# Kernel optimization log

Hardware: AMD Instinct MI355X
Metric: run time of the kernel (lower is better)

## Reference

```python
import jax, jax.numpy as jnp
import numpy as np

EMBED_DIM = 1024
NUM_HEADS = 16
D_K = EMBED_DIM // NUM_HEADS
GAMMA = 1.0


def setup_inputs() -> dict:
    key = jax.random.key(0)
    ks = jax.random.split(key, 5)
    B, N, E = 2, 2048, EMBED_DIM
    scale = 1.0 / np.sqrt(E)
    x = jax.random.normal(ks[0], (B, N, E), dtype=jnp.float32)
    Wq = jax.random.normal(ks[1], (E, E), dtype=jnp.float32) * scale
    Wk = jax.random.normal(ks[2], (E, E), dtype=jnp.float32) * scale
    Wv = jax.random.normal(ks[3], (E, E), dtype=jnp.float32) * scale
    Wo = jax.random.normal(ks[4], (E, E), dtype=jnp.float32) * scale
    mask = jnp.ones((B, N), dtype=jnp.int32)
    return {"x": x, "Wq": Wq, "Wk": Wk, "Wv": Wv, "Wo": Wo, "mask": mask}


def _split_heads(t):
    B, N, E = t.shape
    return t.reshape(B, N, NUM_HEADS, D_K).transpose(0, 2, 1, 3)  # [B,H,N,dk]


def reference(x, Wq, Wk, Wv, Wo, mask):
    B, N, E = x.shape
    # Linear layers (bias=False): y = x @ W.T
    q = _split_heads(x @ Wq.T)
    k = _split_heads(x @ Wk.T)
    v = _split_heads(x @ Wv.T)
    # Squared L2 distance via ||q||^2 + ||k||^2 - 2 q.k (same math as (q-k)^2.sum,
    # without materializing the [B,H,N,N,dk] diff tensor).
    q_sq = jnp.sum(q * q, axis=-1)  # [B,H,N]
    k_sq = jnp.sum(k * k, axis=-1)  # [B,H,N]
    qk = jnp.einsum('bhqd,bhkd->bhqk', q, k)
    sq_dist = jnp.maximum(q_sq[..., :, None] + k_sq[..., None, :] - 2.0 * qk, 0.0)
    similarity = jnp.exp(-GAMMA * sq_dist)  # [B,H,N,N]
    # mask.unsqueeze(1).unsqueeze(2): broadcast over heads and query dim
    mask_exp = mask[:, None, None, :]  # [B,1,1,N]
    similarity = jnp.where(mask_exp == 0, jnp.float32(-1e9), similarity)
    attn = jax.nn.softmax(similarity, axis=-1)
    # dropout p=0.0 (eval) -> identity
    out = jnp.einsum('bhqk,bhkd->bhqd', attn, v)
    out = out.transpose(0, 2, 1, 3).reshape(B, N, E)
    return out @ Wo.T
```

## Files before the change

### kernel.cpp

```cpp
#include <hip/hip_runtime.h>
#include <hip/hip_bf16.h>


using bf16x8 = __attribute__((ext_vector_type(8))) __bf16;
using f32x4  = __attribute__((ext_vector_type(4))) float;
using f32x16 = __attribute__((ext_vector_type(16))) float;

typedef const __attribute__((address_space(1))) void* gas_t;
typedef __attribute__((address_space(3))) void* las_t;

#define C_LOG2E 1.4426950408889634f
#define TWO_C   2.8853900817779268f
#define NEG_INV_4C (-0.17328679513998632f)

#if __has_builtin(__builtin_amdgcn_exp2f)
#define EXP2(x) __builtin_amdgcn_exp2f(x)
#else
#define EXP2(x) __expf((x) * 0.6931471805599453f)
#endif

static __device__ __forceinline__ unsigned short f2bf(float x) {
  union { float f; unsigned u; } c; c.f = x;
  unsigned u = c.u;
  u += 0x7fffu + ((u >> 16) & 1u);
  return (unsigned short)(u >> 16);
}
static __device__ __forceinline__ float bf2f(unsigned short b) {
  union { unsigned u; float f; } c; c.u = ((unsigned)b) << 16;
  return c.f;
}
static __device__ __forceinline__ unsigned cvt_pk_bf16(float lo, float hi) {
  unsigned r;
  asm("v_cvt_pk_bf16_f32 %0, %1, %2" : "=v"(r) : "v"(lo), "v"(hi));
  return r;
}
static __device__ __forceinline__ void permlane32_swap(unsigned &a, unsigned &b) {
#if __has_builtin(__builtin_amdgcn_permlane32_swap)
  auto r = __builtin_amdgcn_permlane32_swap(a, b, false, false);
  a = r[0]; b = r[1];
#else
  asm("v_permlane32_swap_b32 %0, %1" : "+v"(a), "+v"(b));
#endif
}

#define SYNC_VM(N)                                                           \
  do {                                                                       \
    asm volatile("s_waitcnt vmcnt(" #N ") lgkmcnt(0)\n\ts_barrier" ::: "memory"); \
    __builtin_amdgcn_sched_barrier(0);                                       \
  } while (0)

__global__ __launch_bounds__(256)
void cvt_all(const float* __restrict__ x,  const float* __restrict__ wq,
             const float* __restrict__ wk, const float* __restrict__ wv,
             const float* __restrict__ wo,
             unsigned short* __restrict__ xbf, unsigned short* __restrict__ Wbf) {
  const int idx = blockIdx.x * 256 + threadIdx.x;
  const float* src; unsigned short* dst; int off;
  if (idx < 1048576) { src = x; dst = xbf; off = idx; }
  else {
    const int r = idx - 1048576;
    const int w = r >> 18;
    off = r & 262143;
    src = (w == 0) ? wq : (w == 1) ? wk : (w == 2) ? wv : wo;
    dst = Wbf + (size_t)w * 1048576u;
  }
  const float4 v = ((const float4*)src)[off];
  ushort4 o;
  o.x = f2bf(v.x); o.y = f2bf(v.y); o.z = f2bf(v.z); o.w = f2bf(v.w);
  ((ushort4*)dst)[off] = o;
}

__global__ __launch_bounds__(256)
void gemm_bt(const unsigned short* __restrict__ A,
             const unsigned short* __restrict__ Bt,
             void* __restrict__ out0, int Kdim, int mode) {
  __shared__ unsigned short As[3][4096];
  __shared__ unsigned short Bs[3][4096];
  const int t  = threadIdx.x;
  const int m0 = blockIdx.x * 128;
  const int n0 = blockIdx.y * 128;
  const int srow = t >> 2;
  const int scol = (((t & 3) ^ (srow & 3) ^ ((srow >> 2) & 3))) * 8;
  const unsigned short* pA = A  + (size_t)(m0 + srow) * Kdim + scol;
  const unsigned short* pB = Bt + (size_t)(n0 + srow) * Kdim + scol;
  const size_t rowskip = (size_t)64 * Kdim;

  const int wave = t >> 6, lane = t & 63;
  const int wm = (wave >> 1) * 64, wn = (wave & 1) * 64;
  const int fr = lane & 15, fg = lane >> 4;
  const int fswz = fg ^ (fr & 3) ^ ((fr >> 2) & 3);
  const int aoff = (wm + fr) * 32 + fswz * 8;
  const int boff = (wn + fr) * 32 + fswz * 8;

  f32x4 acc[4][4];
#pragma unroll
  for (int mi = 0; mi < 4; ++mi)
#pragma unroll
    for (int ni = 0; ni < 4; ++ni)
      acc[mi][ni] = (f32x4){0.f, 0.f, 0.f, 0.f};

#define GSTAGE(bi, kk)                                                                                  \
  do {                                                                                                  \
    const int kc = (kk) * 32;                                                                           \
    __builtin_amdgcn_global_load_lds((gas_t)(const void*)(pA + kc),           (las_t)(void*)(As[bi] + t * 8),        16, 0, 0); \
    __builtin_amdgcn_global_load_lds((gas_t)(const void*)(pA + kc + rowskip), (las_t)(void*)(As[bi] + 2048 + t * 8), 16, 0, 0); \
    __builtin_amdgcn_global_load_lds((gas_t)(const void*)(pB + kc),           (las_t)(void*)(Bs[bi] + t * 8),        16, 0, 0); \
    __builtin_amdgcn_global_load_lds((gas_t)(const void*)(pB + kc + rowskip), (las_t)(void*)(Bs[bi] + 2048 + t * 8), 16, 0, 0); \
  } while (0)

  const int NK = Kdim >> 5;
  GSTAGE(0, 0);
  GSTAGE(1, 1);

  for (int ks = 0; ks < NK; ++ks) {
    const int cur = ks % 3;
    if (ks + 1 < NK) SYNC_VM(4); else SYNC_VM(0);
    if (ks + 2 < NK) GSTAGE((ks + 2) % 3, ks + 2);

    bf16x8 af[4], bfr[4];
#pragma unroll
    for (int mi = 0; mi < 4; ++mi) af[mi]  = *(const bf16x8*)(As[cur] + aoff + mi * 512);
#pragma unroll
    for (int ni = 0; ni < 4; ++ni) bfr[ni] = *(const bf16x8*)(Bs[cur] + boff + ni * 512);
#pragma unroll
    for (int mi = 0; mi < 4; ++mi)
#pragma unroll
      for (int ni = 0; ni < 4; ++ni)
        acc[mi][ni] = __builtin_amdgcn_mfma_f32_16x16x32_bf16(af[mi], bfr[ni], acc[mi][ni], 0, 0, 0);
  }
#undef GSTAGE

#pragma unroll
  for (int mi = 0; mi < 4; ++mi) {
    const int gm = m0 + wm + mi * 16 + fg * 4;
#pragma unroll
    for (int ni = 0; ni < 4; ++ni) {
      const int gn = n0 + wn + ni * 16 + fr;
      if (mode == 0) {
        unsigned short* outw = (unsigned short*)out0;
        const int z = gn >> 10, col = gn & 1023;
        if (z < 2) {
          const float sc = (z == 0) ? TWO_C : 1.0f;
          unsigned short* dst = outw + (size_t)z * 4194304u;
#pragma unroll
          for (int r = 0; r < 4; ++r)
            dst[(size_t)(gm + r) * 1024 + col] = f2bf(acc[mi][ni][r] * sc);
        } else {
          ushort4 o4;
          o4.x = f2bf(acc[mi][ni][0]); o4.y = f2bf(acc[mi][ni][1]);
          o4.z = f2bf(acc[mi][ni][2]); o4.w = f2bf(acc[mi][ni][3]);
          const int bb = gm >> 11, nn = gm & 2047;
          const int hh = col >> 6, dd = col & 63;
          unsigned short* vt = outw + (size_t)2 * 4194304u;
          *(ushort4*)(vt + ((size_t)((bb * 16 + hh) * 64 + dd)) * 2048 + nn) = o4;
        }
      } else {
        float* dst = (float*)out0;
#pragma unroll
        for (int r = 0; r < 4; ++r)
          dst[(size_t)(gm + r) * 1024 + gn] = acc[mi][ni][r];
      }
    }
  }
}

__global__ __launch_bounds__(256)
void rowsq_kernel(const unsigned short* __restrict__ Qbf,
                  const unsigned short* __restrict__ Kbf,
                  const int* __restrict__ mask,
                  float* __restrict__ qsqp, float* __restrict__ ksqp,
                  float* __restrict__ maskf,
                  float* __restrict__ FullVm,
                  float* __restrict__ den_base,
                  unsigned* __restrict__ kmax_bits) {
  const int tid = blockIdx.x * 256 + threadIdx.x;
  const int kpath = blockIdx.y;
  const unsigned short* src = (kpath == 0) ? Qbf : Kbf;
  const int bh = tid >> 11, n = tid & 2047;
  const int b = bh >> 4, h = bh & 15;
  const unsigned short* row = src + (size_t)(b * 2048 + n) * 1024 + h * 64;
  float s = 0.f;
#pragma unroll
  for (int c = 0; c < 64; c += 4) {
    ushort4 v = *(const ushort4*)(row + c);
    float f0 = bf2f(v.x), f1 = bf2f(v.y), f2 = bf2f(v.z), f3 = bf2f(v.w);
    s += f0 * f0 + f1 * f1 + f2 * f2 + f3 * f3;
  }
  if (kpath == 0) {
    qsqp[tid] = s * NEG_INV_4C;
    if (tid < 2048) FullVm[tid] = 0.f;
    if (tid < 32) kmax_bits[tid] = 0xFF800000u;
    if (tid < 2) den_base[tid] = 0.f;
  } else {
    ksqp[tid] = s * (-C_LOG2E);
    if (tid < 4096) maskf[tid] = (mask[tid] == 0) ? 0.f : 1.f;
  }
}

__global__ __launch_bounds__(256)
void prep2_kernel(const unsigned short* __restrict__ Vt,
                  const float* __restrict__ maskf,
                  const float* __restrict__ ksqp,
                  float* __restrict__ FullVm,
                  float* __restrict__ den_base,
                  unsigned* __restrict__ kmax_bits) {
  const int bh = blockIdx.x, c = blockIdx.y;
  const int b = bh >> 4;
  const int wave = threadIdx.x >> 6, lane = threadIdx.x & 63;
  const int k0 = c * 256;
  const float4 mv = *(const float4*)(maskf + b * 2048 + k0 + lane * 4);
#pragma unroll 4
  for (int dr = wave * 16; dr < wave * 16 + 16; ++dr) {
    const ushort4 v = *(const ushort4*)(Vt + ((size_t)bh * 64 + dr) * 2048 + k0 + lane * 4);
    float s = bf2f(v.x) * mv.x + bf2f(v.y) * mv.y + bf2f(v.z) * mv.z + bf2f(v.w) * mv.w;
#pragma unroll
    for (int off = 32; off >= 1; off >>= 1) s += __shfl_xor(s, off);
    if (lane == 0) atomicAdd(&FullVm[bh * 64 + dr], s);
  }
  if (wave == 0) {
    const float4 kq = *(const float4*)(ksqp + bh * 2048 + k0 + lane * 4);
    float mx = fmaxf(fmaxf(kq.x, kq.y), fmaxf(kq.z, kq.w));
#pragma unroll
    for (int off = 32; off >= 1; off >>= 1) mx = fmaxf(mx, __shfl_xor(mx, off));
    if (lane == 0) atomicMin(&kmax_bits[bh], __float_as_uint(mx));
  }
  if (wave == 1 && (bh & 15) == 0) {
    float s = mv.x + mv.y + mv.z + mv.w;
#pragma unroll
    for (int off = 32; off >= 1; off >>= 1) s += __shfl_xor(s, off);
    if (lane == 0) atomicAdd(&den_base[b], s);
  }
}

__global__ __launch_bounds__(256)
void attn_kernel(const unsigned short* __restrict__ Qbf,
                 const unsigned short* __restrict__ Kbf,
                 const unsigned short* __restrict__ Vt,
                 const float* __restrict__ qsqp,
                 const float* __restrict__ ksqp,
                 const float* __restrict__ maskf,
                 const float* __restrict__ FullVm,
                 const float* __restrict__ den_base,
                 const float* __restrict__ kmaxb,
                 unsigned short* __restrict__ Obf) {
  __shared__ unsigned short Ks[3][8192];

  const int bh = blockIdx.x;
  const int b = bh >> 4, h = bh & 15;
  const int t = threadIdx.x;
  const int wave = t >> 6, lane = t & 63;
  const int qg = wave >> 1, hf = wave & 1;
  const int li = lane & 31, hi = lane >> 5;
  const int q0 = blockIdx.y * 64 + qg * 32;
  const int qrow = q0 + li;

  const unsigned short* Qr = Qbf + (size_t)(b * 2048 + qrow) * 1024 + h * 64 + hi * 8;
  bf16x8 qf[4];
#pragma unroll
  for (int dblk = 0; dblk < 4; ++dblk) qf[dblk] = *(const bf16x8*)(Qr + dblk * 16);

  const float qsl = qsqp[bh * 2048 + qrow];
  const float thr = -14.0f - qsl - kmaxb[bh];

  const unsigned short* Kbase = Kbf + (size_t)b * 2048 * 1024 + h * 64;
  const unsigned short* VtB = Vt + (size_t)bh * 64 * 2048;

  const int p0 = t,       r0 = p0 >> 3, c0 = (p0 & 7) ^ (r0 & 7);
  const int p1 = 256 + t, r1 = p1 >> 3, c1 = (p1 & 7) ^ (r1 & 7);
  const int p2 = 512 + t, r2 = p2 >> 3, c2 = (p2 & 7) ^ (r2 & 7);
  const int p3 = 768 + t, r3 = p3 >> 3, c3 = (p3 & 7) ^ (r3 & 7);

  f32x16 oa0, oa1;
#pragma unroll
  for (int r = 0; r < 16; ++r) { oa0[r] = 0.f; oa1[r] = 0.f; }
  float den = 0.f;

#define STAGE(bi, tj)                                                                               \
  do {                                                                                              \
    const int j0s = (tj) * 128;                                                                     \
    __builtin_amdgcn_global_load_lds((gas_t)(const void*)(Kbase + (size_t)(j0s + r0) * 1024 + c0 * 8), \
                                     (las_t)(void*)(Ks[bi] + p0 * 8), 16, 0, 0);                    \
    __builtin_amdgcn_global_load_lds((gas_t)(const void*)(Kbase + (size_t)(j0s + r1) * 1024 + c1 * 8), \
                                     (las_t)(void*)(Ks[bi] + p1 * 8), 16, 0, 0);                    \
    __builtin_amdgcn_global_load_lds((gas_t)(const void*)(Kbase + (size_t)(j0s + r2) * 1024 + c2 * 8), \
                                     (las_t)(void*)(Ks[bi] + p2 * 8), 16, 0, 0);                    \
    __builtin_amdgcn_global_load_lds((gas_t)(const void*)(Kbase + (size_t)(j0s + r3) * 1024 + c3 * 8), \
                                     (las_t)(void*)(Ks[bi] + p3 * 8), 16, 0, 0);                    \
  } while (0)

  STAGE(0, 0);
  STAGE(1, 1);

  const int jw = hf * 64;
  const int ksw = li & 7;

  auto slow_path = [&](const f32x16& st, int j0s) {
    const float* ksb2 = ksqp + bh * 2048 + j0s + 4 * hi;
    const float* mfb2 = maskf + b * 2048 + j0s + 4 * hi;
    const float4 kq0 = *(const float4*)(ksb2);
    const float4 kq1 = *(const float4*)(ksb2 + 8);
    const float4 kq2 = *(const float4*)(ksb2 + 16);
    const float4 kq3 = *(const float4*)(ksb2 + 24);
    const float4 mf0 = *(const float4*)(mfb2);
    const float4 mf1 = *(const float4*)(mfb2 + 8);
    const float4 mf2 = *(const float4*)(mfb2 + 16);
    const float4 mf3 = *(const float4*)(mfb2 + 24);
    const float kqa[16] = {kq0.x, kq0.y, kq0.z, kq0.w, kq1.x, kq1.y, kq1.z, kq1.w,
                           kq2.x, kq2.y, kq2.z, kq2.w, kq3.x, kq3.y, kq3.z, kq3.w};
    const float mfa[16] = {mf0.x, mf0.y, mf0.z, mf0.w, mf1.x, mf1.y, mf1.z, mf1.w,
                           mf2.x, mf2.y, mf2.z, mf2.w, mf3.x, mf3.y, mf3.z, mf3.w};
    float dsv[16];
#pragma unroll
    for (int r = 0; r < 16; ++r) {
      const float z = __builtin_fminf(st[r] + qsl + kqa[r], 0.f);
      const float s = EXP2(z);
      float pl = __builtin_fmaf(s, 1.f / 120.f, 1.f / 24.f);
      pl = __builtin_fmaf(s, pl, 1.f / 6.f);
      pl = __builtin_fmaf(s, pl, 0.5f);
      pl = __builtin_fmaf(s, pl, 1.f);
      const float d_ = s * pl * mfa[r];
      dsv[r] = d_;
      den += d_;
    }
    unsigned u00 = cvt_pk_bf16(dsv[0],  dsv[1]);
    unsigned u01 = cvt_pk_bf16(dsv[2],  dsv[3]);
    unsigned u10 = cvt_pk_bf16(dsv[4],  dsv[5]);
    unsigned u11 = cvt_pk_bf16(dsv[6],  dsv[7]);
    unsigned u20 = cvt_pk_bf16(dsv[8],  dsv[9]);
    unsigned u21 = cvt_pk_bf16(dsv[10], dsv[11]);
    unsigned u30 = cvt_pk_bf16(dsv[12], dsv[13]);
    unsigned u31 = cvt_pk_bf16(dsv[14], dsv[15]);
    permlane32_swap(u00, u10);
    permlane32_swap(u01, u11);
    permlane32_swap(u20, u30);
    permlane32_swap(u21, u31);
    union { unsigned u[4]; bf16x8 v; } pf0, pf1;
    pf0.u[0] = u00; pf0.u[1] = u01; pf0.u[2] = u10; pf0.u[3] = u11;
    pf1.u[0] = u20; pf1.u[1] = u21; pf1.u[2] = u30; pf1.u[3] = u31;
#pragma unroll
    for (int dh = 0; dh < 2; ++dh) {
      const unsigned short* Vrow = VtB + (size_t)(dh * 32 + li) * 2048 + j0s;
      const bf16x8 vf0 = *(const bf16x8*)(Vrow + hi * 8);
      const bf16x8 vf1 = *(const bf16x8*)(Vrow + 16 + hi * 8);
      if (dh == 0) {
        oa0 = __builtin_amdgcn_mfma_f32_32x32x16_bf16(vf0, pf0.v, oa0, 0, 0, 0);
        oa0 = __builtin_amdgcn_mfma_f32_32x32x16_bf16(vf1, pf1.v, oa0, 0, 0, 0);
      } else {
        oa1 = __builtin_amdgcn_mfma_f32_32x32x16_bf16(vf0, pf0.v, oa1, 0, 0, 0);
        oa1 = __builtin_amdgcn_mfma_f32_32x32x16_bf16(vf1, pf1.v, oa1, 0, 0, 0);
      }
    }
  };

  for (int tj = 0; tj < 16; ++tj) {
    const int cur = tj % 3;
    if (tj + 1 < 16) SYNC_VM(4); else SYNC_VM(0);
    if (tj + 2 < 16) STAGE((tj + 2) % 3, tj + 2);

    const unsigned short* Krow0 = Ks[cur] + (jw + li) * 64;
    const unsigned short* Krow1 = Ks[cur] + (jw + 32 + li) * 64;
    f32x16 st0, st1;
#pragma unroll
    for (int r = 0; r < 16; ++r) { st0[r] = 0.f; st1[r] = 0.f; }
#pragma unroll
    for (int dblk = 0; dblk < 4; ++dblk) {
      const int ch = ((dblk * 2 + hi) ^ ksw) * 8;
      const bf16x8 kf0 = *(const bf16x8*)(Krow0 + ch);
      const bf16x8 kf1 = *(const bf16x8*)(Krow1 + ch);
      st0 = __builtin_amdgcn_mfma_f32_32x32x16_bf16(kf0, qf[dblk], st0, 0, 0, 0);
      st1 = __builtin_amdgcn_mfma_f32_32x32x16_bf16(kf1, qf[dblk], st1, 0, 0, 0);
    }

    const float a0 = fmaxf(fmaxf(st0[0], st0[1]), fmaxf(st0[2], st0[3]));
    const float a1 = fmaxf(fmaxf(st0[4], st0[5]), fmaxf(st0[6], st0[7]));
    const float a2 = fmaxf(fmaxf(st0[8], st0[9]), fmaxf(st0[10], st0[11]));
    const float a3 = fmaxf(fmaxf(st0[12], st0[13]), fmaxf(st0[14], st0[15]));
    const float lmax0 = fmaxf(fmaxf(a0, a1), fmaxf(a2, a3));
    const float b0 = fmaxf(fmaxf(st1[0], st1[1]), fmaxf(st1[2], st1[3]));
    const float b1 = fmaxf(fmaxf(st1[4], st1[5]), fmaxf(st1[6], st1[7]));
    const float b2 = fmaxf(fmaxf(st1[8], st1[9]), fmaxf(st1[10], st1[11]));
    const float b3 = fmaxf(fmaxf(st1[12], st1[13]), fmaxf(st1[14], st1[15]));
    const float lmax1 = fmaxf(fmaxf(b0, b1), fmaxf(b2, b3));

    const int j0 = tj * 128 + jw;
    if (__any(lmax0 > thr)) slow_path(st0, j0);
    if (__any(lmax1 > thr)) slow_path(st1, j0 + 32);
  }
#undef STAGE

  den += __shfl_xor(den, 32);

  __syncthreads();
  float* Obuf = (float*)&Ks[0][0];
  float* Dbuf = (float*)&Ks[0][0] + 4096;
  if (hf == 1) {
#pragma unroll
    for (int r = 0; r < 16; ++r) {
      Obuf[(qg * 32 + r) * 64 + lane]      = oa0[r];
      Obuf[(qg * 32 + 16 + r) * 64 + lane] = oa1[r];
    }
    Dbuf[qg * 64 + lane] = den;
  }
  __syncthreads();
  if (hf == 0) {
    const float inv = 1.f / (den_base[b] + den + Dbuf[qg * 64 + lane]);
    const float* fvm = FullVm + bh * 64;
    unsigned short* orow = Obf + (size_t)(b * 2048 + qrow) * 1024 + h * 64;
#pragma unroll
    for (int dh = 0; dh < 2; ++dh)
#pragma unroll
      for (int w = 0; w < 4; ++w) {
        float v0, v1, v2, v3;
        if (dh == 0) {
          v0 = oa0[4 * w];     v1 = oa0[4 * w + 1];
          v2 = oa0[4 * w + 2]; v3 = oa0[4 * w + 3];
        } else {
          v0 = oa1[4 * w];     v1 = oa1[4 * w + 1];
          v2 = oa1[4 * w + 2]; v3 = oa1[4 * w + 3];
        }
        const int sbase = (qg * 32 + dh * 16 + 4 * w) * 64 + lane;
        v0 += Obuf[sbase];       v1 += Obuf[sbase + 64];
        v2 += Obuf[sbase + 128]; v3 += Obuf[sbase + 192];
        const float4 fv = *(const float4*)(fvm + dh * 32 + w * 8 + hi * 4);
        ushort4 o4;
        o4.x = f2bf((v0 + fv.x) * inv);
        o4.y = f2bf((v1 + fv.y) * inv);
        o4.z = f2bf((v2 + fv.z) * inv);
        o4.w = f2bf((v3 + fv.w) * inv);
        *(ushort4*)(orow + dh * 32 + w * 8 + hi * 4) = o4;
      }
  }
}

extern "C" void kernel_launch(void* const* d_in, const int* in_sizes, int n_in,
                              void* d_out, int out_size, void* d_ws, size_t ws_size,
                              hipStream_t stream) {
  const float* x  = (const float*)d_in[0];
  const float* Wq = (const float*)d_in[1];
  const float* Wk = (const float*)d_in[2];
  const float* Wv = (const float*)d_in[3];
  const float* Wo = (const float*)d_in[4];
  const int* mask = (const int*)d_in[5];

  unsigned short* ws = (unsigned short*)d_ws;
  const size_t SZ = 4194304;
  unsigned short* xbf = ws;
  unsigned short* Wbf = ws + SZ;
  unsigned short* Qbf = ws + 2 * SZ;
  unsigned short* Kbf = ws + 3 * SZ;
  unsigned short* Vt  = ws + 4 * SZ;
  unsigned short* Obf = ws + 5 * SZ;
  float* qsqp = (float*)(ws + 6 * SZ);
  float* ksqp = qsqp + 65536;
  float* maskf = ksqp + 65536;
  float* FullVm = maskf + 4096;
  float* den_base = FullVm + 2048;
  float* kmaxb = den_base + 2;

  cvt_all<<<8192, 256, 0, stream>>>(x, Wq, Wk, Wv, Wo, xbf, Wbf);

  gemm_bt<<<dim3(32, 24), 256, 0, stream>>>(xbf, Wbf, Qbf, 1024, 0);

  rowsq_kernel<<<dim3(256, 2), 256, 0, stream>>>(Qbf, Kbf, mask, qsqp, ksqp, maskf,
                                                 FullVm, den_base, (unsigned*)kmaxb);

  prep2_kernel<<<dim3(32, 8), 256, 0, stream>>>(Vt, maskf, ksqp, FullVm, den_base,
                                                (unsigned*)kmaxb);

  attn_kernel<<<dim3(32, 32), 256, 0, stream>>>(Qbf, Kbf, Vt, qsqp, ksqp, maskf,
                                                FullVm, den_base, kmaxb, Obf);

  gemm_bt<<<dim3(32, 8), 256, 0, stream>>>(Obf, Wbf + 3145728, d_out, 1024, 1);
}
```

Baseline: 117.7 us.

## Merge prep kernels into rowsq and reshape attention waves to share K fragments

The buffer initialisation moves into the conversion kernel, and the prep2 work folds into rowsq as a third grid slice that computes K row norms and the mask itself, so one launch and the dependency between them go away. The attention kernel now has each wave own 32 keys across both 32-row query groups. Each K fragment read from shared memory then feeds two MFMAs, which halves LDS reads per MFMA. The cost is twice the accumulator registers (four 16-float tiles), which may lower occupancy, and a heavier final reduction across four waves through shared memory.

```diff
diff --git a/kernel.cpp b/kernel.cpp
--- a/kernel.cpp
+++ b/kernel.cpp
@@ -53,8 +53,17 @@
 void cvt_all(const float* __restrict__ x,  const float* __restrict__ wq,
              const float* __restrict__ wk, const float* __restrict__ wv,
              const float* __restrict__ wo,
-             unsigned short* __restrict__ xbf, unsigned short* __restrict__ Wbf) {
+             unsigned short* __restrict__ xbf, unsigned short* __restrict__ Wbf,
+             float* __restrict__ FullVm, float* __restrict__ den_base,
+             unsigned* __restrict__ kmax_bits) {
   const int idx = blockIdx.x * 256 + threadIdx.x;
+  if (blockIdx.x == 0) {
+    const int tid = threadIdx.x;
+#pragma unroll
+    for (int i = 0; i < 8; ++i) FullVm[tid + i * 256] = 0.f;
+    if (tid < 32) kmax_bits[tid] = 0xFF800000u;
+    if (tid < 2) den_base[tid] = 0.f;
+  }
   const float* src; unsigned short* dst; int off;
   if (idx < 1048576) { src = x; dst = xbf; off = idx; }
   else {
@@ -167,65 +176,68 @@
 __global__ __launch_bounds__(256)
 void rowsq_kernel(const unsigned short* __restrict__ Qbf,
                   const unsigned short* __restrict__ Kbf,
+                  const unsigned short* __restrict__ Vt,
                   const int* __restrict__ mask,
                   float* __restrict__ qsqp, float* __restrict__ ksqp,
                   float* __restrict__ maskf,
                   float* __restrict__ FullVm,
                   float* __restrict__ den_base,
                   unsigned* __restrict__ kmax_bits) {
-  const int tid = blockIdx.x * 256 + threadIdx.x;
   const int kpath = blockIdx.y;
-  const unsigned short* src = (kpath == 0) ? Qbf : Kbf;
-  const int bh = tid >> 11, n = tid & 2047;
-  const int b = bh >> 4, h = bh & 15;
-  const unsigned short* row = src + (size_t)(b * 2048 + n) * 1024 + h * 64;
-  float s = 0.f;
-#pragma unroll
-  for (int c = 0; c < 64; c += 4) {
-    ushort4 v = *(const ushort4*)(row + c);
-    float f0 = bf2f(v.x), f1 = bf2f(v.y), f2 = bf2f(v.z), f3 = bf2f(v.w);
-    s += f0 * f0 + f1 * f1 + f2 * f2 + f3 * f3;
-  }
-  if (kpath == 0) {
-    qsqp[tid] = s * NEG_INV_4C;
-    if (tid < 2048) FullVm[tid] = 0.f;
-    if (tid < 32) kmax_bits[tid] = 0xFF800000u;
-    if (tid < 2) den_base[tid] = 0.f;
-  } else {
-    ksqp[tid] = s * (-C_LOG2E);
-    if (tid < 4096) maskf[tid] = (mask[tid] == 0) ? 0.f : 1.f;
-  }
-}
-
-__global__ __launch_bounds__(256)
-void prep2_kernel(const unsigned short* __restrict__ Vt,
-                  const float* __restrict__ maskf,
-                  const float* __restrict__ ksqp,
-                  float* __restrict__ FullVm,
-                  float* __restrict__ den_base,
-                  unsigned* __restrict__ kmax_bits) {
-  const int bh = blockIdx.x, c = blockIdx.y;
+  if (kpath < 2) {
+    const int tid = blockIdx.x * 256 + threadIdx.x;
+    const unsigned short* src = (kpath == 0) ? Qbf : Kbf;
+    const int bh = tid >> 11, n = tid & 2047;
+    const int b = bh >> 4, h = bh & 15;
+    const unsigned short* row = src + (size_t)(b * 2048 + n) * 1024 + h * 64;
+    float s = 0.f;
+#pragma unroll
+    for (int c = 0; c < 64; c += 4) {
+      ushort4 v = *(const ushort4*)(row + c);
+      float f0 = bf2f(v.x), f1 = bf2f(v.y), f2 = bf2f(v.z), f3 = bf2f(v.w);
+      s += f0 * f0 + f1 * f1 + f2 * f2 + f3 * f3;
+    }
+    if (kpath == 0) {
+      qsqp[tid] = s * NEG_INV_4C;
+    } else {
+      ksqp[tid] = s * (-C_LOG2E);
+      if (tid < 4096) maskf[tid] = (mask[tid] == 0) ? 0.f : 1.f;
+    }
+    return;
+  }
+  const int bh = blockIdx.x >> 3, c = blockIdx.x & 7;
   const int b = bh >> 4;
   const int wave = threadIdx.x >> 6, lane = threadIdx.x & 63;
   const int k0 = c * 256;
-  const float4 mv = *(const float4*)(maskf + b * 2048 + k0 + lane * 4);
+  const int4 mi4 = *(const int4*)(mask + b * 2048 + k0 + lane * 4);
+  const float mvx = mi4.x ? 1.f : 0.f, mvy = mi4.y ? 1.f : 0.f;
+  const float mvz = mi4.z ? 1.f : 0.f, mvw = mi4.w ? 1.f : 0.f;
 #pragma unroll 4
   for (int dr = wave * 16; dr < wave * 16 + 16; ++dr) {
     const ushort4 v = *(const ushort4*)(Vt + ((size_t)bh * 64 + dr) * 2048 + k0 + lane * 4);
-    float s = bf2f(v.x) * mv.x + bf2f(v.y) * mv.y + bf2f(v.z) * mv.z + bf2f(v.w) * mv.w;
+    float s = bf2f(v.x) * mvx + bf2f(v.y) * mvy + bf2f(v.z) * mvz + bf2f(v.w) * mvw;
 #pragma unroll
     for (int off = 32; off >= 1; off >>= 1) s += __shfl_xor(s, off);
     if (lane == 0) atomicAdd(&FullVm[bh * 64 + dr], s);
   }
-  if (wave == 0) {
-    const float4 kq = *(const float4*)(ksqp + bh * 2048 + k0 + lane * 4);
-    float mx = fmaxf(fmaxf(kq.x, kq.y), fmaxf(kq.z, kq.w));
+  {
+    const int h = bh & 15;
+    const int krow = k0 + wave * 64 + lane;
+    const unsigned short* row = Kbf + (size_t)(b * 2048 + krow) * 1024 + h * 64;
+    float s = 0.f;
+#pragma unroll
+    for (int cc = 0; cc < 64; cc += 4) {
+      ushort4 v = *(const ushort4*)(row + cc);
+      float f0 = bf2f(v.x), f1 = bf2f(v.y), f2 = bf2f(v.z), f3 = bf2f(v.w);
+      s += f0 * f0 + f1 * f1 + f2 * f2 + f3 * f3;
+    }
+    float mx = s * (-C_LOG2E);
 #pragma unroll
     for (int off = 32; off >= 1; off >>= 1) mx = fmaxf(mx, __shfl_xor(mx, off));
     if (lane == 0) atomicMin(&kmax_bits[bh], __float_as_uint(mx));
   }
-  if (wave == 1 && (bh & 15) == 0) {
-    float s = mv.x + mv.y + mv.z + mv.w;
+  if (wave == 3 && (bh & 15) == 0) {
+    float s = mvx + mvy + mvz + mvw;
 #pragma unroll
     for (int off = 32; off >= 1; off >>= 1) s += __shfl_xor(s, off);
     if (lane == 0) atomicAdd(&den_base[b], s);
@@ -244,23 +256,30 @@
                  const float* __restrict__ kmaxb,
                  unsigned short* __restrict__ Obf) {
   __shared__ unsigned short Ks[3][8192];
+  __shared__ float Dbuf2[3][2][64];
 
   const int bh = blockIdx.x;
   const int b = bh >> 4, h = bh & 15;
   const int t = threadIdx.x;
   const int wave = t >> 6, lane = t & 63;
-  const int qg = wave >> 1, hf = wave & 1;
   const int li = lane & 31, hi = lane >> 5;
-  const int q0 = blockIdx.y * 64 + qg * 32;
-  const int qrow = q0 + li;
-
-  const unsigned short* Qr = Qbf + (size_t)(b * 2048 + qrow) * 1024 + h * 64 + hi * 8;
-  bf16x8 qf[4];
-#pragma unroll
-  for (int dblk = 0; dblk < 4; ++dblk) qf[dblk] = *(const bf16x8*)(Qr + dblk * 16);
-
-  const float qsl = qsqp[bh * 2048 + qrow];
-  const float thr = -14.0f - qsl - kmaxb[bh];
+  const int q0 = blockIdx.y * 64;
+  const int qrow0 = q0 + li, qrow1 = q0 + 32 + li;
+
+  const unsigned short* Qr0 = Qbf + (size_t)(b * 2048 + qrow0) * 1024 + h * 64 + hi * 8;
+  const unsigned short* Qr1 = Qbf + (size_t)(b * 2048 + qrow1) * 1024 + h * 64 + hi * 8;
+  bf16x8 qf0[4], qf1[4];
+#pragma unroll
+  for (int dblk = 0; dblk < 4; ++dblk) {
+    qf0[dblk] = *(const bf16x8*)(Qr0 + dblk * 16);
+    qf1[dblk] = *(const bf16x8*)(Qr1 + dblk * 16);
+  }
+
+  const float qsl0 = qsqp[bh * 2048 + qrow0];
+  const float qsl1 = qsqp[bh * 2048 + qrow1];
+  const float kmx = kmaxb[bh];
+  const float thr0 = -14.0f - qsl0 - kmx;
+  const float thr1 = -14.0f - qsl1 - kmx;
 
   const unsigned short* Kbase = Kbf + (size_t)b * 2048 * 1024 + h * 64;
   const unsigned short* VtB = Vt + (size_t)bh * 64 * 2048;
@@ -270,10 +289,10 @@
   const int p2 = 512 + t, r2 = p2 >> 3, c2 = (p2 & 7) ^ (r2 & 7);
   const int p3 = 768 + t, r3 = p3 >> 3, c3 = (p3 & 7) ^ (r3 & 7);
 
-  f32x16 oa0, oa1;
-#pragma unroll
-  for (int r = 0; r < 16; ++r) { oa0[r] = 0.f; oa1[r] = 0.f; }
-  float den = 0.f;
+  f32x16 oa00, oa01, oa10, oa11;
+#pragma unroll
+  for (int r = 0; r < 16; ++r) { oa00[r] = 0.f; oa01[r] = 0.f; oa10[r] = 0.f; oa11[r] = 0.f; }
+  float den0 = 0.f, den1 = 0.f;
 
 #define STAGE(bi, tj)                                                                               \
   do {                                                                                              \
@@ -291,84 +310,81 @@
   STAGE(0, 0);
   STAGE(1, 1);
 
-  const int jw = hf * 64;
   const int ksw = li & 7;
 
-  auto slow_path = [&](const f32x16& st, int j0s) {
-    const float* ksb2 = ksqp + bh * 2048 + j0s + 4 * hi;
-    const float* mfb2 = maskf + b * 2048 + j0s + 4 * hi;
-    const float4 kq0 = *(const float4*)(ksb2);
-    const float4 kq1 = *(const float4*)(ksb2 + 8);
-    const float4 kq2 = *(const float4*)(ksb2 + 16);
-    const float4 kq3 = *(const float4*)(ksb2 + 24);
-    const float4 mf0 = *(const float4*)(mfb2);
-    const float4 mf1 = *(const float4*)(mfb2 + 8);
-    const float4 mf2 = *(const float4*)(mfb2 + 16);
-    const float4 mf3 = *(const float4*)(mfb2 + 24);
-    const float kqa[16] = {kq0.x, kq0.y, kq0.z, kq0.w, kq1.x, kq1.y, kq1.z, kq1.w,
-                           kq2.x, kq2.y, kq2.z, kq2.w, kq3.x, kq3.y, kq3.z, kq3.w};
-    const float mfa[16] = {mf0.x, mf0.y, mf0.z, mf0.w, mf1.x, mf1.y, mf1.z, mf1.w,
-                           mf2.x, mf2.y, mf2.z, mf2.w, mf3.x, mf3.y, mf3.z, mf3.w};
-    float dsv[16];
-#pragma unroll
-    for (int r = 0; r < 16; ++r) {
-      const float z = __builtin_fminf(st[r] + qsl + kqa[r], 0.f);
-      const float s = EXP2(z);
-      float pl = __builtin_fmaf(s, 1.f / 120.f, 1.f / 24.f);
-      pl = __builtin_fmaf(s, pl, 1.f / 6.f);
-      pl = __builtin_fmaf(s, pl, 0.5f);
-      pl = __builtin_fmaf(s, pl, 1.f);
-      const float d_ = s * pl * mfa[r];
-      dsv[r] = d_;
-      den += d_;
-    }
-    unsigned u00 = cvt_pk_bf16(dsv[0],  dsv[1]);
-    unsigned u01 = cvt_pk_bf16(dsv[2],  dsv[3]);
-    unsigned u10 = cvt_pk_bf16(dsv[4],  dsv[5]);
-    unsigned u11 = cvt_pk_bf16(dsv[6],  dsv[7]);
-    unsigned u20 = cvt_pk_bf16(dsv[8],  dsv[9]);
-    unsigned u21 = cvt_pk_bf16(dsv[10], dsv[11]);
-    unsigned u30 = cvt_pk_bf16(dsv[12], dsv[13]);
-    unsigned u31 = cvt_pk_bf16(dsv[14], dsv[15]);
-    permlane32_swap(u00, u10);
-    permlane32_swap(u01, u11);
-    permlane32_swap(u20, u30);
-    permlane32_swap(u21, u31);
-    union { unsigned u[4]; bf16x8 v; } pf0, pf1;
-    pf0.u[0] = u00; pf0.u[1] = u01; pf0.u[2] = u10; pf0.u[3] = u11;
-    pf1.u[0] = u20; pf1.u[1] = u21; pf1.u[2] = u30; pf1.u[3] = u31;
-#pragma unroll
-    for (int dh = 0; dh < 2; ++dh) {
-      const unsigned short* Vrow = VtB + (size_t)(dh * 32 + li) * 2048 + j0s;
-      const bf16x8 vf0 = *(const bf16x8*)(Vrow + hi * 8);
-      const bf16x8 vf1 = *(const bf16x8*)(Vrow + 16 + hi * 8);
-      if (dh == 0) {
-        oa0 = __builtin_amdgcn_mfma_f32_32x32x16_bf16(vf0, pf0.v, oa0, 0, 0, 0);
-        oa0 = __builtin_amdgcn_mfma_f32_32x32x16_bf16(vf1, pf1.v, oa0, 0, 0, 0);
-      } else {
-        oa1 = __builtin_amdgcn_mfma_f32_32x32x16_bf16(vf0, pf0.v, oa1, 0, 0, 0);
-        oa1 = __builtin_amdgcn_mfma_f32_32x32x16_bf16(vf1, pf1.v, oa1, 0, 0, 0);
-      }
-    }
-  };
+#define SLOWP(ST, QSLH, J0S, OA_A, OA_B, DENH)                                   \
+  do {                                                                           \
+    const float* ksb2 = ksqp + bh * 2048 + (J0S) + 4 * hi;                       \
+    const float* mfb2 = maskf + b * 2048 + (J0S) + 4 * hi;                       \
+    const float4 kq0 = *(const float4*)(ksb2);                                   \
+    const float4 kq1 = *(const float4*)(ksb2 + 8);                               \
+    const float4 kq2 = *(const float4*)(ksb2 + 16);                              \
+    const float4 kq3 = *(const float4*)(ksb2 + 24);                              \
+    const float4 mf0 = *(const float4*)(mfb2);                                   \
+    const float4 mf1 = *(const float4*)(mfb2 + 8);                               \
+    const float4 mf2 = *(const float4*)(mfb2 + 16);                              \
+    const float4 mf3 = *(const float4*)(mfb2 + 24);                              \
+    const float kqa[16] = {kq0.x, kq0.y, kq0.z, kq0.w, kq1.x, kq1.y, kq1.z, kq1.w, \
+                           kq2.x, kq2.y, kq2.z, kq2.w, kq3.x, kq3.y, kq3.z, kq3.w}; \
+    const float mfa[16] = {mf0.x, mf0.y, mf0.z, mf0.w, mf1.x, mf1.y, mf1.z, mf1.w, \
+                           mf2.x, mf2.y, mf2.z, mf2.w, mf3.x, mf3.y, mf3.z, mf3.w}; \
+    float dsv[16];                                                               \
+    _Pragma("unroll")                                                            \
+    for (int r = 0; r < 16; ++r) {                                               \
+      const float z = __builtin_fminf((ST)[r] + (QSLH) + kqa[r], 0.f);           \
+      const float s = EXP2(z);                                                   \
+      float pl = __builtin_fmaf(s, 1.f / 120.f, 1.f / 24.f);                     \
+      pl = __builtin_fmaf(s, pl, 1.f / 6.f);                                     \
+      pl = __builtin_fmaf(s, pl, 0.5f);                                          \
+      pl = __builtin_fmaf(s, pl, 1.f);                                           \
+      const float d_ = s * pl * mfa[r];                                          \
+      dsv[r] = d_;                                                               \
+      (DENH) += d_;                                                              \
+    }                                                                            \
+    unsigned u00 = cvt_pk_bf16(dsv[0],  dsv[1]);                                 \
+    unsigned u01 = cvt_pk_bf16(dsv[2],  dsv[3]);                                 \
+    unsigned u10 = cvt_pk_bf16(dsv[4],  dsv[5]);                                 \
+    unsigned u11 = cvt_pk_bf16(dsv[6],  dsv[7]);                                 \
+    unsigned u20 = cvt_pk_bf16(dsv[8],  dsv[9]);                                 \
+    unsigned u21 = cvt_pk_bf16(dsv[10], dsv[11]);                                \
+    unsigned u30 = cvt_pk_bf16(dsv[12], dsv[13]);                                \
+    unsigned u31 = cvt_pk_bf16(dsv[14], dsv[15]);                                \
+    permlane32_swap(u00, u10);                                                   \
+    permlane32_swap(u01, u11);                                                   \
+    permlane32_swap(u20, u30);                                                   \
+    permlane32_swap(u21, u31);                                                   \
+    union { unsigned u[4]; bf16x8 v; } pf0, pf1;                                 \
+    pf0.u[0] = u00; pf0.u[1] = u01; pf0.u[2] = u10; pf0.u[3] = u11;              \
+    pf1.u[0] = u20; pf1.u[1] = u21; pf1.u[2] = u30; pf1.u[3] = u31;              \
+    _Pragma("unroll")                                                            \
+    for (int dh = 0; dh < 2; ++dh) {                                             \
+      const unsigned short* Vrow = VtB + (size_t)(dh * 32 + li) * 2048 + (J0S);  \
+      const bf16x8 vfa = *(const bf16x8*)(Vrow + hi * 8);                        \
+      const bf16x8 vfb = *(const bf16x8*)(Vrow + 16 + hi * 8);                   \
+      if (dh == 0) {                                                             \
+        (OA_A) = __builtin_amdgcn_mfma_f32_32x32x16_bf16(vfa, pf0.v, (OA_A), 0, 0, 0); \
+        (OA_A) = __builtin_amdgcn_mfma_f32_32x32x16_bf16(vfb, pf1.v, (OA_A), 0, 0, 0); \
+      } else {                                                                   \
+        (OA_B) = __builtin_amdgcn_mfma_f32_32x32x16_bf16(vfa, pf0.v, (OA_B), 0, 0, 0); \
+        (OA_B) = __builtin_amdgcn_mfma_f32_32x32x16_bf16(vfb, pf1.v, (OA_B), 0, 0, 0); \
+      }                                                                          \
+    }                                                                            \
+  } while (0)
 
   for (int tj = 0; tj < 16; ++tj) {
     const int cur = tj % 3;
     if (tj + 1 < 16) SYNC_VM(4); else SYNC_VM(0);
     if (tj + 2 < 16) STAGE((tj + 2) % 3, tj + 2);
 
-    const unsigned short* Krow0 = Ks[cur] + (jw + li) * 64;
-    const unsigned short* Krow1 = Ks[cur] + (jw + 32 + li) * 64;
+    const unsigned short* Krow = Ks[cur] + (wave * 32 + li) * 64;
     f32x16 st0, st1;
 #pragma unroll
     for (int r = 0; r < 16; ++r) { st0[r] = 0.f; st1[r] = 0.f; }
 #pragma unroll
     for (int dblk = 0; dblk < 4; ++dblk) {
-      const int ch = ((dblk * 2 + hi) ^ ksw) * 8;
-      const bf16x8 kf0 = *(const bf16x8*)(Krow0 + ch);
-      const bf16x8 kf1 = *(const bf16x8*)(Krow1 + ch);
-      st0 = __builtin_amdgcn_mfma_f32_32x32x16_bf16(kf0, qf[dblk], st0, 0, 0, 0);
-      st1 = __builtin_amdgcn_mfma_f32_32x32x16_bf16(kf1, qf[dblk], st1, 0, 0, 0);
+      const bf16x8 kf = *(const bf16x8*)(Krow + ((dblk * 2 + hi) ^ ksw) * 8);
+      st0 = __builtin_amdgcn_mfma_f32_32x32x16_bf16(kf, qf0[dblk], st0, 0, 0, 0);
+      st1 = __builtin_amdgcn_mfma_f32_32x32x16_bf16(kf, qf1[dblk], st1, 0, 0, 0);
     }
 
     const float a0 = fmaxf(fmaxf(st0[0], st0[1]), fmaxf(st0[2], st0[3]));
@@ -382,53 +398,69 @@
     const float b3 = fmaxf(fmaxf(st1[12], st1[13]), fmaxf(st1[14], st1[15]));
     const float lmax1 = fmaxf(fmaxf(b0, b1), fmaxf(b2, b3));
 
-    const int j0 = tj * 128 + jw;
-    if (__any(lmax0 > thr)) slow_path(st0, j0);
-    if (__any(lmax1 > thr)) slow_path(st1, j0 + 32);
+    const int j0 = tj * 128 + wave * 32;
+    if (__any(lmax0 > thr0)) SLOWP(st0, qsl0, j0, oa00, oa01, den0);
+    if (__any(lmax1 > thr1)) SLOWP(st1, qsl1, j0, oa10, oa11, den1);
   }
 #undef STAGE
-
-  den += __shfl_xor(den, 32);
+#undef SLOWP
+
+  den0 += __shfl_xor(den0, 32);
+  den1 += __shfl_xor(den1, 32);
 
   __syncthreads();
   float* Obuf = (float*)&Ks[0][0];
-  float* Dbuf = (float*)&Ks[0][0] + 4096;
-  if (hf == 1) {
+  if (wave > 0) {
+    const int wb = (wave - 1) * 4096;
 #pragma unroll
     for (int r = 0; r < 16; ++r) {
-      Obuf[(qg * 32 + r) * 64 + lane]      = oa0[r];
-      Obuf[(qg * 32 + 16 + r) * 64 + lane] = oa1[r];
-    }
-    Dbuf[qg * 64 + lane] = den;
+      Obuf[wb + (0 * 16 + r) * 64 + lane] = oa00[r];
+      Obuf[wb + (1 * 16 + r) * 64 + lane] = oa01[r];
+      Obuf[wb + (2 * 16 + r) * 64 + lane] = oa10[r];
+      Obuf[wb + (3 * 16 + r) * 64 + lane] = oa11[r];
+    }
+    Dbuf2[wave - 1][0][lane] = den0;
+    Dbuf2[wave - 1][1][lane] = den1;
   }
   __syncthreads();
-  if (hf == 0) {
-    const float inv = 1.f / (den_base[b] + den + Dbuf[qg * 64 + lane]);
+  if (wave == 0) {
+#pragma unroll
+    for (int w2 = 0; w2 < 3; ++w2) {
+      const int wb = w2 * 4096;
+#pragma unroll
+      for (int r = 0; r < 16; ++r) {
+        oa00[r] += Obuf[wb + (0 * 16 + r) * 64 + lane];
+        oa01[r] += Obuf[wb + (1 * 16 + r) * 64 + lane];
+        oa10[r] += Obuf[wb + (2 * 16 + r) * 64 + lane];
+        oa11[r] += Obuf[wb + (3 * 16 + r) * 64 + lane];
+      }
+      den0 += Dbuf2[w2][0][lane];
+      den1 += Dbuf2[w2][1][lane];
+    }
+    const float dbase = den_base[b];
     const float* fvm = FullVm + bh * 64;
-    unsigned short* orow = Obf + (size_t)(b * 2048 + qrow) * 1024 + h * 64;
-#pragma unroll
-    for (int dh = 0; dh < 2; ++dh)
-#pragma unroll
-      for (int w = 0; w < 4; ++w) {
-        float v0, v1, v2, v3;
-        if (dh == 0) {
-          v0 = oa0[4 * w];     v1 = oa0[4 * w + 1];
-          v2 = oa0[4 * w + 2]; v3 = oa0[4 * w + 3];
-        } else {
-          v0 = oa1[4 * w];     v1 = oa1[4 * w + 1];
-          v2 = oa1[4 * w + 2]; v3 = oa1[4 * w + 3];
+#pragma unroll
+    for (int qh = 0; qh < 2; ++qh) {
+      const float inv = 1.f / (dbase + (qh == 0 ? den0 : den1));
+      unsigned short* orow = Obf + (size_t)(b * 2048 + q0 + qh * 32 + li) * 1024 + h * 64;
+#pragma unroll
+      for (int dh = 0; dh < 2; ++dh)
+#pragma unroll
+        for (int w = 0; w < 4; ++w) {
+          float v0, v1, v2, v3;
+          if (qh == 0 && dh == 0)      { v0 = oa00[4*w]; v1 = oa00[4*w+1]; v2 = oa00[4*w+2]; v3 = oa00[4*w+3]; }
+          else if (qh == 0 && dh == 1) { v0 = oa01[4*w]; v1 = oa01[4*w+1]; v2 = oa01[4*w+2]; v3 = oa01[4*w+3]; }
+          else if (qh == 1 && dh == 0) { v0 = oa10[4*w]; v1 = oa10[4*w+1]; v2 = oa10[4*w+2]; v3 = oa10[4*w+3]; }
+          else                         { v0 = oa11[4*w]; v1 = oa11[4*w+1]; v2 = oa11[4*w+2]; v3 = oa11[4*w+3]; }
+          const float4 fv = *(const float4*)(fvm + dh * 32 + w * 8 + hi * 4);
+          ushort4 o4;
+          o4.x = f2bf((v0 + fv.x) * inv);
+          o4.y = f2bf((v1 + fv.y) * inv);
+          o4.z = f2bf((v2 + fv.z) * inv);
+          o4.w = f2bf((v3 + fv.w) * inv);
+          *(ushort4*)(orow + dh * 32 + w * 8 + hi * 4) = o4;
         }
-        const int sbase = (qg * 32 + dh * 16 + 4 * w) * 64 + lane;
-        v0 += Obuf[sbase];       v1 += Obuf[sbase + 64];
-        v2 += Obuf[sbase + 128]; v3 += Obuf[sbase + 192];
-        const float4 fv = *(const float4*)(fvm + dh * 32 + w * 8 + hi * 4);
-        ushort4 o4;
-        o4.x = f2bf((v0 + fv.x) * inv);
-        o4.y = f2bf((v1 + fv.y) * inv);
-        o4.z = f2bf((v2 + fv.z) * inv);
-        o4.w = f2bf((v3 + fv.w) * inv);
-        *(ushort4*)(orow + dh * 32 + w * 8 + hi * 4) = o4;
-      }
+    }
   }
 }
 
@@ -457,15 +489,14 @@
   float* den_base = FullVm + 2048;
   float* kmaxb = den_base + 2;
 
-  cvt_all<<<8192, 256, 0, stream>>>(x, Wq, Wk, Wv, Wo, xbf, Wbf);
+  cvt_all<<<8192, 256, 0, stream>>>(x, Wq, Wk, Wv, Wo, xbf, Wbf,
+                                    FullVm, den_base, (unsigned*)kmaxb);
 
   gemm_bt<<<dim3(32, 24), 256, 0, stream>>>(xbf, Wbf, Qbf, 1024, 0);
 
-  rowsq_kernel<<<dim3(256, 2), 256, 0, stream>>>(Qbf, Kbf, mask, qsqp, ksqp, maskf,
-                                                 FullVm, den_base, (unsigned*)kmaxb);
-
-  prep2_kernel<<<dim3(32, 8), 256, 0, stream>>>(Vt, maskf, ksqp, FullVm, den_base,
-                                                (unsigned*)kmaxb);
+  rowsq_kernel<<<dim3(256, 3), 256, 0, stream>>>(Qbf, Kbf, Vt, mask, qsqp, ksqp,
+                                                 maskf, FullVm, den_base,
+                                                 (unsigned*)kmaxb);
 
   attn_kernel<<<dim3(32, 32), 256, 0, stream>>>(Qbf, Kbf, Vt, qsqp, ksqp, maskf,
                                                 FullVm, den_base, kmaxb, Obf);
```

New measurement: 149.8 us. 27.3% more time.
